# Kernel optimization log

Measured on AMD Instinct MI355X. Metric: run time of the kernel, lower is better.

## Reference

```python
import jax, jax.numpy as jnp
import numpy as np
from jax import lax

B, S, I = 128, 256, 128          # batch, seq_len, input_size
CTX, OUT = 256, 128              # context_input_size, output_size
CPM, NM = 1024, 4                # center_size_per_module, num_modules
CENTER = NM * CPM
IN_SIZES = [I + CTX, CTX, CTX, CTX]          # only module 0 sees the input
HID = [CPM, CPM, CPM, CPM + OUT]             # last module also emits output


def setup_inputs() -> dict:
    key = jax.random.key(0)
    ks = jax.random.split(key, 4 + 5 * NM)
    d = {
        "inputs": jax.random.normal(ks[0], (B, 1, S, I), jnp.float32),
        "center_init": jax.random.normal(ks[1], (NM, B, CPM), jnp.float32),
        "mod_init": jax.random.normal(ks[2], (NM - 1, B, CPM), jnp.float32),
        "mod_init_last": jax.random.normal(ks[3], (B, CPM + OUT), jnp.float32),
    }
    for i in range(NM):
        k = ks[4 + 5 * i: 4 + 5 * (i + 1)]
        d[f"pm{i}"] = jax.random.normal(k[0], (CENTER, CTX), jnp.float32) * 0.02
        d[f"wih{i}"] = jax.random.normal(k[1], (3 * HID[i], IN_SIZES[i]), jnp.float32) * 0.05
        d[f"whh{i}"] = jax.random.normal(k[2], (3 * HID[i], HID[i]), jnp.float32) * 0.05
        d[f"bih{i}"] = jnp.zeros((3 * HID[i],), jnp.float32)
        d[f"bhh{i}"] = jnp.zeros((3 * HID[i],), jnp.float32)
    return d


def _gru(x, h, wih, whh, bih, bhh):
    # PyTorch GRUCell semantics
    gi = x @ wih.T + bih
    gh = h @ whh.T + bhh
    ir, iz, inn = jnp.split(gi, 3, axis=1)
    hr, hz, hn = jnp.split(gh, 3, axis=1)
    r = jax.nn.sigmoid(ir + hr)
    z = jax.nn.sigmoid(iz + hz)
    n = jnp.tanh(inn + r * hn)
    return (1.0 - z) * n + z * h


def _forward(inputs, center_init, mod_init, mod_init_last, pms, wihs, whhs, bihs, bhhs):
    xs = jnp.swapaxes(inputs[:, 0], 0, 1)  # [S, B, I]

    def step(carry, x_t):
        centers, mods, mod_last = carry  # [NM,B,CPM], [NM-1,B,CPM], [B,CPM+OUT]
        # torch.cat(prev_center_states, dim=1): module-major concat -> [B, NM*CPM]
        center_state = jnp.reshape(jnp.swapaxes(centers, 0, 1), (centers.shape[1], -1))
        new_centers, new_mods = [], []
        out = new_mod_last = None
        for i in range(NM):
            ctx = center_state @ pms[i]                       # [B, CTX]
            xin = jnp.concatenate([x_t, ctx], axis=1) if i == 0 else ctx
            h_prev = mod_last if i == NM - 1 else mods[i]
            h = _gru(xin, h_prev, wihs[i], whhs[i], bihs[i], bhhs[i])
            if i == NM - 1:
                out = h[:, :OUT]                              # split([output, center_feat])
                new_centers.append(h[:, OUT:])
                new_mod_last = h
            else:
                new_centers.append(h)
                new_mods.append(h)
        return (jnp.stack(new_centers), jnp.stack(new_mods), new_mod_last), out

    _, ys = lax.scan(step, (center_init, mod_init, mod_init_last), xs)
    return jnp.swapaxes(ys, 0, 1)  # [B, S, OUT]


def reference(inputs, center_init, mod_init, mod_init_last,
              pm0, pm1, pm2, pm3,
              wih0, wih1, wih2, wih3,
              whh0, whh1, whh2, whh3,
              bih0, bih1, bih2, bih3,
              bhh0, bhh1, bhh2, bhh3):
    return _forward(inputs, center_init, mod_init, mod_init_last,
                    (pm0, pm1, pm2, pm3),
                    (wih0, wih1, wih2, wih3),
                    (whh0, whh1, whh2, whh3),
                    (bih0, bih1, bih2, bih3),
                    (bhh0, bhh1, bhh2, bhh3))
```

## Files before the change

### kernel.cpp

```cpp
#include <hip/hip_runtime.h>
#include <hip/hip_bf16.h>

typedef _Float16 f16;
typedef f16  f16x8 __attribute__((ext_vector_type(8)));
typedef float f32x4 __attribute__((ext_vector_type(4)));

__device__ __forceinline__ f16x8 ld8h(const f16* p){ return *reinterpret_cast<const f16x8*>(p); }
__device__ __forceinline__ void fsplit(float x, f16* hi, f16* lo){
    f16 h=(f16)x; *hi=h; *lo=(f16)((x-(float)h)*4096.0f);
}
#define MFMA16(a,b,c) __builtin_amdgcn_mfma_f32_16x16x32_f16((a),(b),(c),0,0,0)
__device__ __forceinline__ size_t fragoff(int n, int k, int Kc){
    return ((size_t)(n>>4)*Kc + (k>>5))*512 + (size_t)((((k&31)>>3)*16 + (n&15))*8 + (k&7));
}

constexpr size_t NXE   = 128ull*256*128;
constexpr size_t NPM   = 1024ull*4096;
constexpr size_t NWIH0 = 3072ull*384;
constexpr size_t NWIH12= 3072ull*256;
constexpr size_t NWIH3 = 3456ull*256;
constexpr size_t NWHH  = 3072ull*1024;
constexpr size_t NWHH3 = 3456ull*1152;
constexpr size_t NCEN  = 128ull*4096;
constexpr size_t NCTX  = 128ull*1024;
constexpr size_t NHMX  = 128ull*1152;

constexpr size_t OFF_XH    = 0;
constexpr size_t OFF_XL    = OFF_XH + NXE*2;
constexpr size_t OFF_PMH   = OFF_XL + NXE*2;
constexpr size_t OFF_PML   = OFF_PMH + NPM*2;
constexpr size_t OFF_WIHH0 = OFF_PML + NPM*2;
constexpr size_t OFF_WIHH1 = OFF_WIHH0 + NWIH0*2;
constexpr size_t OFF_WIHH2 = OFF_WIHH1 + NWIH12*2;
constexpr size_t OFF_WIHH3 = OFF_WIHH2 + NWIH12*2;
constexpr size_t OFF_WIHL0 = OFF_WIHH3 + NWIH3*2;
constexpr size_t OFF_WIHL1 = OFF_WIHL0 + NWIH0*2;
constexpr size_t OFF_WIHL2 = OFF_WIHL1 + NWIH12*2;
constexpr size_t OFF_WIHL3 = OFF_WIHL2 + NWIH12*2;
constexpr size_t OFF_WHHH0 = OFF_WIHL3 + NWIH3*2;
constexpr size_t OFF_WHHH1 = OFF_WHHH0 + NWHH*2;
constexpr size_t OFF_WHHH2 = OFF_WHHH1 + NWHH*2;
constexpr size_t OFF_WHHH3 = OFF_WHHH2 + NWHH*2;
constexpr size_t OFF_WHHL0 = OFF_WHHH3 + NWHH3*2;
constexpr size_t OFF_WHHL1 = OFF_WHHL0 + NWHH*2;
constexpr size_t OFF_WHHL2 = OFF_WHHL1 + NWHH*2;
constexpr size_t OFF_WHHL3 = OFF_WHHL2 + NWHH*2;
constexpr size_t OFF_CENH  = OFF_WHHL3 + NWHH3*2;
constexpr size_t OFF_CENL  = OFF_CENH + 2*NCEN*2;
constexpr size_t OFF_CTXH  = OFF_CENL + 2*NCEN*2;
constexpr size_t OFF_CTXL  = OFF_CTXH + NCTX*2;
constexpr size_t OFF_HH    = OFF_CTXL + NCTX*2;
constexpr size_t OFF_HL    = OFF_HH + 8*NHMX*2;
constexpr size_t OFF_HF    = OFF_HL + 8*NHMX*2;
constexpr size_t WS_NEED   = OFF_HF + 8*NHMX*4;

__device__ __forceinline__ f16* hh_ptr(char* ws,int p,int i){ return (f16*)(ws+OFF_HH+((size_t)(p*4+i))*NHMX*2); }
__device__ __forceinline__ f16* hl_ptr(char* ws,int p,int i){ return (f16*)(ws+OFF_HL+((size_t)(p*4+i))*NHMX*2); }
__device__ __forceinline__ float* hf_ptr(char* ws,int p,int i){ return (float*)(ws+OFF_HF+((size_t)(p*4+i))*NHMX*4); }

__global__ void k_repack_w(const float* __restrict__ src, f16* __restrict__ hi,
                           f16* __restrict__ lo, int K){
    int n = blockIdx.x;
    const float* row = src + (size_t)n*K;
    int Kc = K >> 5;
    for (int k8 = threadIdx.x*8; k8 < K; k8 += 2048) {
        f16x8 hv, lv;
        #pragma unroll
        for (int e = 0; e < 8; ++e) { f16 a,b; fsplit(row[k8+e], &a, &b); hv[e]=a; lv[e]=b; }
        size_t d = fragoff(n, k8, Kc);
        *reinterpret_cast<f16x8*>(hi + d) = hv;
        *reinterpret_cast<f16x8*>(lo + d) = lv;
    }
}

__global__ void k_repack_pm(const float* __restrict__ p0, const float* __restrict__ p1,
                            const float* __restrict__ p2, const float* __restrict__ p3,
                            f16* __restrict__ hi, f16* __restrict__ lo){
    int k0 = blockIdx.x * 8;
    for (int c = threadIdx.x; c < 1024; c += 256) {
        int i = c >> 8, nl = c & 255;
        const float* p = (i==0?p0 : i==1?p1 : i==2?p2 : p3);
        #pragma unroll
        for (int e = 0; e < 8; ++e) {
            f16 a,b; fsplit(p[(size_t)(k0+e)*256 + nl], &a, &b);
            size_t d = fragoff(c, k0+e, 128); hi[d]=a; lo[d]=b;
        }
    }
}

__global__ void k_repack_x(const float* __restrict__ src, f16* __restrict__ hi, f16* __restrict__ lo){
    size_t g = ((size_t)blockIdx.x*256 + threadIdx.x) * 8;
    if (g >= NXE) return;
    int m = (int)(g >> 15), t = (int)((g >> 7) & 255), d0 = (int)(g & 127);
    f16x8 hv, lv;
    #pragma unroll
    for (int e = 0; e < 8; ++e) { f16 a,b; fsplit(src[g+e], &a, &b); hv[e]=a; lv[e]=b; }
    size_t d = (size_t)t*16384 + fragoff(m, d0, 4);
    *reinterpret_cast<f16x8*>(hi + d) = hv;
    *reinterpret_cast<f16x8*>(lo + d) = lv;
}

__global__ void k_init_cen(const float* __restrict__ ci, char* ws){
    size_t g = ((size_t)blockIdx.x*256 + threadIdx.x) * 8;
    if (g >= 4ull*128*1024) return;
    int i = (int)(g >> 17), b = (int)((g >> 10) & 127), c = (int)(g & 1023);
    f16* hi = (f16*)(ws + OFF_CENH);
    f16* lo = (f16*)(ws + OFF_CENL);
    f16x8 hv, lv;
    #pragma unroll
    for (int e = 0; e < 8; ++e) { f16 a,bb; fsplit(ci[g+e], &a, &bb); hv[e]=a; lv[e]=bb; }
    size_t d = fragoff(b, i*1024 + c, 128);
    *reinterpret_cast<f16x8*>(hi + d) = hv;
    *reinterpret_cast<f16x8*>(lo + d) = lv;
}

__global__ void k_init_mod(const float* __restrict__ mi, char* ws){
    size_t g = ((size_t)blockIdx.x*256 + threadIdx.x) * 8;
    if (g >= 3ull*128*1024) return;
    int i = (int)(g >> 17), b = (int)((g >> 10) & 127), j = (int)(g & 1023);
    float* hf = hf_ptr(ws, 0, i);
    f16 *hh = hh_ptr(ws, 0, i), *hl = hl_ptr(ws, 0, i);
    f16x8 hv, lv;
    #pragma unroll
    for (int e = 0; e < 8; ++e) {
        float v = mi[g+e]; hf[(size_t)b*1024 + j + e] = v;
        f16 a,bb; fsplit(v, &a, &bb); hv[e]=a; lv[e]=bb;
    }
    size_t d = fragoff(b, j, 32);
    *reinterpret_cast<f16x8*>(hh + d) = hv;
    *reinterpret_cast<f16x8*>(hl + d) = lv;
}

__global__ void k_init_last(const float* __restrict__ ml, char* ws){
    int b = blockIdx.x;
    float* hf = hf_ptr(ws, 0, 3);
    f16 *hh = hh_ptr(ws, 0, 3), *hl = hl_ptr(ws, 0, 3);
    for (int j = threadIdx.x*8; j < 1152; j += 2048) {
        f16x8 hv, lv;
        #pragma unroll
        for (int e = 0; e < 8; ++e) {
            float v = ml[(size_t)b*1152 + j + e]; hf[(size_t)b*1152 + j + e] = v;
            f16 a,bb; fsplit(v, &a, &bb); hv[e]=a; lv[e]=bb;
        }
        size_t d = fragoff(b, j, 36);
        *reinterpret_cast<f16x8*>(hh + d) = hv;
        *reinterpret_cast<f16x8*>(hl + d) = lv;
    }
}

__global__ __launch_bounds__(512) void k_ctx(char* ws, int par){
    __shared__ float red[8][32][17];
    const f16* cenh = (const f16*)(ws + OFF_CENH) + (size_t)par*NCEN;
    const f16* cenl = (const f16*)(ws + OFF_CENL) + (size_t)par*NCEN;
    const f16* pmh  = (const f16*)(ws + OFF_PMH);
    const f16* pml  = (const f16*)(ws + OFF_PML);
    int tid = threadIdx.x, lane = tid & 63, wv = tid >> 6;
    int bm = blockIdx.x >> 6, bn = blockIdx.x & 63;
    size_t lb = (size_t)lane*8;
    size_t a0 = ((size_t)(bm*2)*128 + wv*16)*512 + lb;
    size_t a1 = a0 + 128*512;
    size_t bb = ((size_t)bn*128 + wv*16)*512 + lb;
    f32x4 h0={},h1={},c0={},c1={};
    #pragma unroll 4
    for (int kc = 0; kc < 16; ++kc) {
        f16x8 bh = ld8h(pmh + bb + kc*512), bl = ld8h(pml + bb + kc*512);
        f16x8 ah0 = ld8h(cenh + a0 + kc*512), al0 = ld8h(cenl + a0 + kc*512);
        f16x8 ah1 = ld8h(cenh + a1 + kc*512), al1 = ld8h(cenl + a1 + kc*512);
        h0 = MFMA16(ah0,bh,h0); c0 = MFMA16(al0,bh,c0); c0 = MFMA16(ah0,bl,c0);
        h1 = MFMA16(ah1,bh,h1); c1 = MFMA16(al1,bh,c1); c1 = MFMA16(ah1,bl,c1);
    }
    int rg = lane >> 4, fr = lane & 15;
    const float inv = 1.0f/4096.0f;
    #pragma unroll
    for (int rr = 0; rr < 4; ++rr) {
        red[wv][rg*4+rr][fr]      = h0[rr] + c0[rr]*inv;
        red[wv][16+rg*4+rr][fr]   = h1[rr] + c1[rr]*inv;
    }
    __syncthreads();
    int r = tid >> 4, c = tid & 15;
    float s = red[0][r][c]+red[1][r][c]+red[2][r][c]+red[3][r][c]
            + red[4][r][c]+red[5][r][c]+red[6][r][c]+red[7][r][c];
    int m = bm*32 + r, n = bn*16 + c;
    size_t d = fragoff(m, n, 32);
    f16* ctxh = (f16*)(ws + OFF_CTXH);
    f16* ctxl = (f16*)(ws + OFF_CTXL);
    fsplit(s, &ctxh[d], &ctxl[d]);
}

__global__ __launch_bounds__(512, 2) void k_fused(char* ws,
    const float* __restrict__ bih0, const float* __restrict__ bih1,
    const float* __restrict__ bih2, const float* __restrict__ bih3,
    const float* __restrict__ bhh0, const float* __restrict__ bhh1,
    const float* __restrict__ bhh2, const float* __restrict__ bhh3,
    float* __restrict__ out, int t, int par)
{
    __shared__ float red[8][4][16][17];
    const int tid = threadIdx.x, lane = tid & 63, wv = tid >> 6;
    const int mp = wv & 3, khalf = wv >> 2;
    const int fr = lane & 15, rg = lane >> 4;
    const int tile = blockIdx.x;
    int i, jt;
    if (tile < 64)       { i = 0; jt = tile; }
    else if (tile < 128) { i = 1; jt = tile - 64; }
    else if (tile < 192) { i = 2; jt = tile - 128; }
    else                 { i = 3; jt = tile - 192; }
    const int H  = (i == 3) ? 1152 : 1024;
    const int K1 = (i == 0) ? 384 : 256;
    const int Kc1 = K1 >> 5, KcH = H >> 5, Ht = H >> 4;
    const int P1h = Kc1 >> 1, PHh = KcH >> 1;

    const f16* WihH = (const f16*)(ws + (i==0?OFF_WIHH0 : i==1?OFF_WIHH1 : i==2?OFF_WIHH2 : OFF_WIHH3));
    const f16* WihL = (const f16*)(ws + (i==0?OFF_WIHL0 : i==1?OFF_WIHL1 : i==2?OFF_WIHL2 : OFF_WIHL3));
    const f16* WhhH = (const f16*)(ws + (i==0?OFF_WHHH0 : i==1?OFF_WHHH1 : i==2?OFF_WHHH2 : OFF_WHHH3));
    const f16* WhhL = (const f16*)(ws + (i==0?OFF_WHHL0 : i==1?OFF_WHHL1 : i==2?OFF_WHHL2 : OFF_WHHL3));

    const size_t lb = (size_t)lane*8;
    size_t b1[3], b2[3];
    #pragma unroll
    for (int s = 0; s < 3; ++s) {
        b1[s] = ((size_t)(s*Ht + jt)*Kc1)*512 + lb;
        b2[s] = ((size_t)(s*Ht + jt)*KcH)*512 + lb;
    }
    const int mt0 = mp*2;

    f32x4 aRh[2]={{},{}}, aRc[2]={{},{}}, aZh[2]={{},{}}, aZc[2]={{},{}};
    f32x4 aIh[2]={{},{}}, aIc[2]={{},{}}, aNh[2]={{},{}}, aNc[2]={{},{}};

    {
        const f16* XH_ = (const f16*)(ws + OFF_XH);
        const f16* XL_ = (const f16*)(ws + OFF_XL);
        const f16* CH_ = (const f16*)(ws + OFF_CTXH);
        const f16* CL_ = (const f16*)(ws + OFF_CTXL);
        size_t xb0 = ((size_t)(t*8 + mt0)*4)*512 + lb, xb1 = xb0 + 2048;
        size_t cb0 = ((size_t)mt0*32)*512 + lb,        cb1 = cb0 + 16384;
        const int kc0 = khalf*P1h, kc1e = kc0 + P1h;
        #pragma unroll 2
        for (int kc = kc0; kc < kc1e; ++kc) {
            f16x8 ah0, al0, ah1, al1;
            if (i == 0 && kc < 4) {
                ah0 = ld8h(XH_ + xb0 + kc*512); al0 = ld8h(XL_ + xb0 + kc*512);
                ah1 = ld8h(XH_ + xb1 + kc*512); al1 = ld8h(XL_ + xb1 + kc*512);
            } else {
                const int ck = (i == 0) ? kc - 4 : i*8 + kc;
                ah0 = ld8h(CH_ + cb0 + ck*512); al0 = ld8h(CL_ + cb0 + ck*512);
                ah1 = ld8h(CH_ + cb1 + ck*512); al1 = ld8h(CL_ + cb1 + ck*512);
            }
            f16x8 bh, bl;
            bh = ld8h(WihH + b1[0] + kc*512); bl = ld8h(WihL + b1[0] + kc*512);
            aRh[0]=MFMA16(ah0,bh,aRh[0]); aRc[0]=MFMA16(al0,bh,aRc[0]); aRc[0]=MFMA16(ah0,bl,aRc[0]);
            aRh[1]=MFMA16(ah1,bh,aRh[1]); aRc[1]=MFMA16(al1,bh,aRc[1]); aRc[1]=MFMA16(ah1,bl,aRc[1]);
            bh = ld8h(WihH + b1[1] + kc*512); bl = ld8h(WihL + b1[1] + kc*512);
            aZh[0]=MFMA16(ah0,bh,aZh[0]); aZc[0]=MFMA16(al0,bh,aZc[0]); aZc[0]=MFMA16(ah0,bl,aZc[0]);
            aZh[1]=MFMA16(ah1,bh,aZh[1]); aZc[1]=MFMA16(al1,bh,aZc[1]); aZc[1]=MFMA16(ah1,bl,aZc[1]);
            bh = ld8h(WihH + b1[2] + kc*512); bl = ld8h(WihL + b1[2] + kc*512);
            aIh[0]=MFMA16(ah0,bh,aIh[0]); aIc[0]=MFMA16(al0,bh,aIc[0]); aIc[0]=MFMA16(ah0,bl,aIc[0]);
            aIh[1]=MFMA16(ah1,bh,aIh[1]); aIc[1]=MFMA16(al1,bh,aIc[1]); aIc[1]=MFMA16(ah1,bl,aIc[1]);
        }
    }
    {
        const f16* HHp = hh_ptr(ws, par, i);
        const f16* HLp = hl_ptr(ws, par, i);
        size_t hb0 = ((size_t)mt0*KcH)*512 + lb, hb1 = hb0 + (size_t)KcH*512;
        const int kc0 = khalf*PHh, kc1e = kc0 + PHh;
        #pragma unroll 2
        for (int kc = kc0; kc < kc1e; ++kc) {
            f16x8 ah0 = ld8h(HHp + hb0 + kc*512), al0 = ld8h(HLp + hb0 + kc*512);
            f16x8 ah1 = ld8h(HHp + hb1 + kc*512), al1 = ld8h(HLp + hb1 + kc*512);
            f16x8 bh, bl;
            bh = ld8h(WhhH + b2[0] + kc*512); bl = ld8h(WhhL + b2[0] + kc*512);
            aRh[0]=MFMA16(ah0,bh,aRh[0]); aRc[0]=MFMA16(al0,bh,aRc[0]); aRc[0]=MFMA16(ah0,bl,aRc[0]);
            aRh[1]=MFMA16(ah1,bh,aRh[1]); aRc[1]=MFMA16(al1,bh,aRc[1]); aRc[1]=MFMA16(ah1,bl,aRc[1]);
            bh = ld8h(WhhH + b2[1] + kc*512); bl = ld8h(WhhL + b2[1] + kc*512);
            aZh[0]=MFMA16(ah0,bh,aZh[0]); aZc[0]=MFMA16(al0,bh,aZc[0]); aZc[0]=MFMA16(ah0,bl,aZc[0]);
            aZh[1]=MFMA16(ah1,bh,aZh[1]); aZc[1]=MFMA16(al1,bh,aZc[1]); aZc[1]=MFMA16(ah1,bl,aZc[1]);
            bh = ld8h(WhhH + b2[2] + kc*512); bl = ld8h(WhhL + b2[2] + kc*512);
            aNh[0]=MFMA16(ah0,bh,aNh[0]); aNc[0]=MFMA16(al0,bh,aNc[0]); aNc[0]=MFMA16(ah0,bl,aNc[0]);
            aNh[1]=MFMA16(ah1,bh,aNh[1]); aNc[1]=MFMA16(al1,bh,aNc[1]); aNc[1]=MFMA16(ah1,bl,aNc[1]);
        }
    }

    const float inv = 1.0f/4096.0f;
    if (khalf == 1) {
        #pragma unroll
        for (int mi = 0; mi < 2; ++mi) {
            const int mt = mt0 + mi, r16 = rg*4;
            #pragma unroll
            for (int rr = 0; rr < 4; ++rr) {
                red[mt][0][r16+rr][fr] = aRh[mi][rr] + aRc[mi][rr]*inv;
                red[mt][1][r16+rr][fr] = aZh[mi][rr] + aZc[mi][rr]*inv;
                red[mt][2][r16+rr][fr] = aIh[mi][rr] + aIc[mi][rr]*inv;
                red[mt][3][r16+rr][fr] = aNh[mi][rr] + aNc[mi][rr]*inv;
            }
        }
    }
    __syncthreads();
    if (khalf == 1) return;

    const float* bihp = (i==0?bih0 : i==1?bih1 : i==2?bih2 : bih3);
    const float* bhhp = (i==0?bhh0 : i==1?bhh1 : i==2?bhh2 : bhh3);
    const int j = jt*16 + fr;
    const float bir = bihp[j], biz = bihp[H+j], bin = bihp[2*H+j];
    const float bhr = bhhp[j], bhz = bhhp[H+j], bhn = bhhp[2*H+j];
    const float* hfP = hf_ptr(ws, par, i);
    float* hfN = hf_ptr(ws, par^1, i);
    f16 *hhN = hh_ptr(ws, par^1, i), *hlN = hl_ptr(ws, par^1, i);
    f16* cenhN = (f16*)(ws + OFF_CENH) + (size_t)(par^1)*NCEN;
    f16* cenlN = (f16*)(ws + OFF_CENL) + (size_t)(par^1)*NCEN;
    #pragma unroll
    for (int mi = 0; mi < 2; ++mi) {
        const int mt = mt0 + mi, r16 = rg*4;
        #pragma unroll
        for (int rr = 0; rr < 4; ++rr) {
            float r_  = aRh[mi][rr] + aRc[mi][rr]*inv + red[mt][0][r16+rr][fr] + bir + bhr;
            float z_  = aZh[mi][rr] + aZc[mi][rr]*inv + red[mt][1][r16+rr][fr] + biz + bhz;
            float in_ = aIh[mi][rr] + aIc[mi][rr]*inv + red[mt][2][r16+rr][fr] + bin;
            float hn_ = aNh[mi][rr] + aNc[mi][rr]*inv + red[mt][3][r16+rr][fr] + bhn;
            float rgt = 1.f/(1.f + expf(-r_));
            float zgt = 1.f/(1.f + expf(-z_));
            float ngt = tanhf(in_ + rgt*hn_);
            int m = mt*16 + rg*4 + rr;
            float hp = hfP[(size_t)m*H + j];
            float hnew = (1.f - zgt)*ngt + zgt*hp;
            hfN[(size_t)m*H + j] = hnew;
            size_t hd = fragoff(m, j, KcH);
            fsplit(hnew, &hhN[hd], &hlN[hd]);
            if (i < 3) {
                size_t cd = fragoff(m, i*1024 + j, 128);
                fsplit(hnew, &cenhN[cd], &cenlN[cd]);
            } else if (j >= 128) {
                size_t cd = fragoff(m, 3072 + j - 128, 128);
                fsplit(hnew, &cenhN[cd], &cenlN[cd]);
            } else {
                out[((size_t)m*256 + t)*128 + j] = hnew;
            }
        }
    }
}

extern "C" void kernel_launch(void* const* d_in, const int* in_sizes, int n_in,
                              void* d_out, int out_size, void* d_ws, size_t ws_size,
                              hipStream_t stream)
{
    char* ws = (char*)d_ws;
    const float* inp   = (const float*)d_in[0];
    const float* cini  = (const float*)d_in[1];
    const float* mini  = (const float*)d_in[2];
    const float* mlast = (const float*)d_in[3];
    const float *pm[4], *wih[4], *whh[4], *bih[4], *bhh[4];
    for (int i = 0; i < 4; ++i) {
        pm[i]  = (const float*)d_in[4 + 5*i];
        wih[i] = (const float*)d_in[5 + 5*i];
        whh[i] = (const float*)d_in[6 + 5*i];
        bih[i] = (const float*)d_in[7 + 5*i];
        bhh[i] = (const float*)d_in[8 + 5*i];
    }
    float* out = (float*)d_out;

    k_repack_x<<<2048, 256, 0, stream>>>(inp, (f16*)(ws+OFF_XH), (f16*)(ws+OFF_XL));
    k_repack_pm<<<512, 256, 0, stream>>>(pm[0], pm[1], pm[2], pm[3],
                                         (f16*)(ws+OFF_PMH), (f16*)(ws+OFF_PML));
    k_repack_w<<<3072, 256, 0, stream>>>(wih[0], (f16*)(ws+OFF_WIHH0), (f16*)(ws+OFF_WIHL0), 384);
    k_repack_w<<<3072, 256, 0, stream>>>(wih[1], (f16*)(ws+OFF_WIHH1), (f16*)(ws+OFF_WIHL1), 256);
    k_repack_w<<<3072, 256, 0, stream>>>(wih[2], (f16*)(ws+OFF_WIHH2), (f16*)(ws+OFF_WIHL2), 256);
    k_repack_w<<<3456, 256, 0, stream>>>(wih[3], (f16*)(ws+OFF_WIHH3), (f16*)(ws+OFF_WIHL3), 256);
    k_repack_w<<<3072, 256, 0, stream>>>(whh[0], (f16*)(ws+OFF_WHHH0), (f16*)(ws+OFF_WHHL0), 1024);
    k_repack_w<<<3072, 256, 0, stream>>>(whh[1], (f16*)(ws+OFF_WHHH1), (f16*)(ws+OFF_WHHL1), 1024);
    k_repack_w<<<3072, 256, 0, stream>>>(whh[2], (f16*)(ws+OFF_WHHH2), (f16*)(ws+OFF_WHHL2), 1024);
    k_repack_w<<<3456, 256, 0, stream>>>(whh[3], (f16*)(ws+OFF_WHHH3), (f16*)(ws+OFF_WHHL3), 1152);
    k_init_cen<<<256, 256, 0, stream>>>(cini, ws);
    k_init_mod<<<192, 256, 0, stream>>>(mini, ws);
    k_init_last<<<128, 256, 0, stream>>>(mlast, ws);

    for (int t = 0; t < 256; ++t) {
        int par = t & 1;
        k_ctx<<<256, 512, 0, stream>>>(ws, par);
        k_fused<<<264, 512, 0, stream>>>(ws,
            bih[0], bih[1], bih[2], bih[3],
            bhh[0], bhh[1], bhh[2], bhh[3],
            out, t, par);
    }
    (void)in_sizes; (void)n_in; (void)out_size; (void)ws_size; (void)WS_NEED;
}
```

Before: 12.60 ms.

## Split fused GRU kernel across batch halves and four-way K split

```diff
diff --git a/kernel.cpp b/kernel.cpp
--- a/kernel.cpp
+++ b/kernel.cpp
@@ -187,18 +187,18 @@
     fsplit(s, &ctxh[d], &ctxl[d]);
 }
 
-__global__ __launch_bounds__(512, 2) void k_fused(char* ws,
+__global__ __launch_bounds__(512, 4) void k_fused(char* ws,
     const float* __restrict__ bih0, const float* __restrict__ bih1,
     const float* __restrict__ bih2, const float* __restrict__ bih3,
     const float* __restrict__ bhh0, const float* __restrict__ bhh1,
     const float* __restrict__ bhh2, const float* __restrict__ bhh3,
     float* __restrict__ out, int t, int par)
 {
-    __shared__ float red[8][4][16][17];
+    __shared__ float red[4][4][16][17];
     const int tid = threadIdx.x, lane = tid & 63, wv = tid >> 6;
-    const int mp = wv & 3, khalf = wv >> 2;
+    const int mp = wv & 1, kq = wv >> 1;
     const int fr = lane & 15, rg = lane >> 4;
-    const int tile = blockIdx.x;
+    const int tile = blockIdx.x >> 1, rh = blockIdx.x & 1;
     int i, jt;
     if (tile < 64)       { i = 0; jt = tile; }
     else if (tile < 128) { i = 1; jt = tile - 64; }
@@ -207,7 +207,7 @@
     const int H  = (i == 3) ? 1152 : 1024;
     const int K1 = (i == 0) ? 384 : 256;
     const int Kc1 = K1 >> 5, KcH = H >> 5, Ht = H >> 4;
-    const int P1h = Kc1 >> 1, PHh = KcH >> 1;
+    const int P1q = Kc1 >> 2, PHq = KcH >> 2;
 
     const f16* WihH = (const f16*)(ws + (i==0?OFF_WIHH0 : i==1?OFF_WIHH1 : i==2?OFF_WIHH2 : OFF_WIHH3));
     const f16* WihL = (const f16*)(ws + (i==0?OFF_WIHL0 : i==1?OFF_WIHL1 : i==2?OFF_WIHL2 : OFF_WIHL3));
@@ -221,7 +221,7 @@
         b1[s] = ((size_t)(s*Ht + jt)*Kc1)*512 + lb;
         b2[s] = ((size_t)(s*Ht + jt)*KcH)*512 + lb;
     }
-    const int mt0 = mp*2;
+    const int mt0 = rh*4 + mp*2;
 
     f32x4 aRh[2]={{},{}}, aRc[2]={{},{}}, aZh[2]={{},{}}, aZc[2]={{},{}};
     f32x4 aIh[2]={{},{}}, aIc[2]={{},{}}, aNh[2]={{},{}}, aNc[2]={{},{}};
@@ -233,7 +233,7 @@
         const f16* CL_ = (const f16*)(ws + OFF_CTXL);
         size_t xb0 = ((size_t)(t*8 + mt0)*4)*512 + lb, xb1 = xb0 + 2048;
         size_t cb0 = ((size_t)mt0*32)*512 + lb,        cb1 = cb0 + 16384;
-        const int kc0 = khalf*P1h, kc1e = kc0 + P1h;
+        const int kc0 = kq*P1q, kc1e = kc0 + P1q;
         #pragma unroll 2
         for (int kc = kc0; kc < kc1e; ++kc) {
             f16x8 ah0, al0, ah1, al1;
@@ -261,7 +261,7 @@
         const f16* HHp = hh_ptr(ws, par, i);
         const f16* HLp = hl_ptr(ws, par, i);
         size_t hb0 = ((size_t)mt0*KcH)*512 + lb, hb1 = hb0 + (size_t)KcH*512;
-        const int kc0 = khalf*PHh, kc1e = kc0 + PHh;
+        const int kc0 = kq*PHq, kc1e = kc0 + PHq;
         #pragma unroll 2
         for (int kc = kc0; kc < kc1e; ++kc) {
             f16x8 ah0 = ld8h(HHp + hb0 + kc*512), al0 = ld8h(HLp + hb0 + kc*512);
@@ -280,21 +280,50 @@
     }
 
     const float inv = 1.0f/4096.0f;
-    if (khalf == 1) {
+    const int r16 = rg*4;
+    if (kq == 3) {
         #pragma unroll
         for (int mi = 0; mi < 2; ++mi) {
-            const int mt = mt0 + mi, r16 = rg*4;
+            const int lm = mp*2 + mi;
             #pragma unroll
             for (int rr = 0; rr < 4; ++rr) {
-                red[mt][0][r16+rr][fr] = aRh[mi][rr] + aRc[mi][rr]*inv;
-                red[mt][1][r16+rr][fr] = aZh[mi][rr] + aZc[mi][rr]*inv;
-                red[mt][2][r16+rr][fr] = aIh[mi][rr] + aIc[mi][rr]*inv;
-                red[mt][3][r16+rr][fr] = aNh[mi][rr] + aNc[mi][rr]*inv;
+                red[lm][0][r16+rr][fr] = aRh[mi][rr] + aRc[mi][rr]*inv;
+                red[lm][1][r16+rr][fr] = aZh[mi][rr] + aZc[mi][rr]*inv;
+                red[lm][2][r16+rr][fr] = aIh[mi][rr] + aIc[mi][rr]*inv;
+                red[lm][3][r16+rr][fr] = aNh[mi][rr] + aNc[mi][rr]*inv;
             }
         }
     }
     __syncthreads();
-    if (khalf == 1) return;
+    if (kq == 2) {
+        #pragma unroll
+        for (int mi = 0; mi < 2; ++mi) {
+            const int lm = mp*2 + mi;
+            #pragma unroll
+            for (int rr = 0; rr < 4; ++rr) {
+                red[lm][0][r16+rr][fr] += aRh[mi][rr] + aRc[mi][rr]*inv;
+                red[lm][1][r16+rr][fr] += aZh[mi][rr] + aZc[mi][rr]*inv;
+                red[lm][2][r16+rr][fr] += aIh[mi][rr] + aIc[mi][rr]*inv;
+                red[lm][3][r16+rr][fr] += aNh[mi][rr] + aNc[mi][rr]*inv;
+            }
+        }
+    }
+    __syncthreads();
+    if (kq == 1) {
+        #pragma unroll
+        for (int mi = 0; mi < 2; ++mi) {
+            const int lm = mp*2 + mi;
+            #pragma unroll
+            for (int rr = 0; rr < 4; ++rr) {
+                red[lm][0][r16+rr][fr] += aRh[mi][rr] + aRc[mi][rr]*inv;
+                red[lm][1][r16+rr][fr] += aZh[mi][rr] + aZc[mi][rr]*inv;
+                red[lm][2][r16+rr][fr] += aIh[mi][rr] + aIc[mi][rr]*inv;
+                red[lm][3][r16+rr][fr] += aNh[mi][rr] + aNc[mi][rr]*inv;
+            }
+        }
+    }
+    __syncthreads();
+    if (kq != 0) return;
 
     const float* bihp = (i==0?bih0 : i==1?bih1 : i==2?bih2 : bih3);
     const float* bhhp = (i==0?bhh0 : i==1?bhh1 : i==2?bhh2 : bhh3);
@@ -308,17 +337,17 @@
     f16* cenlN = (f16*)(ws + OFF_CENL) + (size_t)(par^1)*NCEN;
     #pragma unroll
     for (int mi = 0; mi < 2; ++mi) {
-        const int mt = mt0 + mi, r16 = rg*4;
+        const int lm = mp*2 + mi;
         #pragma unroll
         for (int rr = 0; rr < 4; ++rr) {
-            float r_  = aRh[mi][rr] + aRc[mi][rr]*inv + red[mt][0][r16+rr][fr] + bir + bhr;
-            float z_  = aZh[mi][rr] + aZc[mi][rr]*inv + red[mt][1][r16+rr][fr] + biz + bhz;
-            float in_ = aIh[mi][rr] + aIc[mi][rr]*inv + red[mt][2][r16+rr][fr] + bin;
-            float hn_ = aNh[mi][rr] + aNc[mi][rr]*inv + red[mt][3][r16+rr][fr] + bhn;
+            float r_  = aRh[mi][rr] + aRc[mi][rr]*inv + red[lm][0][r16+rr][fr] + bir + bhr;
+            float z_  = aZh[mi][rr] + aZc[mi][rr]*inv + red[lm][1][r16+rr][fr] + biz + bhz;
+            float in_ = aIh[mi][rr] + aIc[mi][rr]*inv + red[lm][2][r16+rr][fr] + bin;
+            float hn_ = aNh[mi][rr] + aNc[mi][rr]*inv + red[lm][3][r16+rr][fr] + bhn;
             float rgt = 1.f/(1.f + expf(-r_));
             float zgt = 1.f/(1.f + expf(-z_));
             float ngt = tanhf(in_ + rgt*hn_);
-            int m = mt*16 + rg*4 + rr;
+            int m = (mt0 + mi)*16 + r16 + rr;
             float hp = hfP[(size_t)m*H + j];
             float hnew = (1.f - zgt)*ngt + zgt*hp;
             hfN[(size_t)m*H + j] = hnew;
@@ -374,7 +403,7 @@
     for (int t = 0; t < 256; ++t) {
         int par = t & 1;
         k_ctx<<<256, 512, 0, stream>>>(ws, par);
-        k_fused<<<264, 512, 0, stream>>>(ws,
+        k_fused<<<528, 512, 0, stream>>>(ws,
             bih[0], bih[1], bih[2], bih[3],
             bhh[0], bhh[1], bhh[2], bhh[3],
             out, t, par);
```

New measurement: 16.56 ms. 1.31x slower.

## Drop separate center and fp32 state buffers; split GRU tiles across more blocks

Applied to the files above, without the earlier changes.

```diff
diff --git a/kernel.cpp b/kernel.cpp
--- a/kernel.cpp
+++ b/kernel.cpp
@@ -21,7 +21,6 @@
 constexpr size_t NWIH3 = 3456ull*256;
 constexpr size_t NWHH  = 3072ull*1024;
 constexpr size_t NWHH3 = 3456ull*1152;
-constexpr size_t NCEN  = 128ull*4096;
 constexpr size_t NCTX  = 128ull*1024;
 constexpr size_t NHMX  = 128ull*1152;
 
@@ -45,18 +44,16 @@
 constexpr size_t OFF_WHHL1 = OFF_WHHL0 + NWHH*2;
 constexpr size_t OFF_WHHL2 = OFF_WHHL1 + NWHH*2;
 constexpr size_t OFF_WHHL3 = OFF_WHHL2 + NWHH*2;
-constexpr size_t OFF_CENH  = OFF_WHHL3 + NWHH3*2;
-constexpr size_t OFF_CENL  = OFF_CENH + 2*NCEN*2;
-constexpr size_t OFF_CTXH  = OFF_CENL + 2*NCEN*2;
+constexpr size_t OFF_C0H   = OFF_WHHL3 + NWHH3*2;
+constexpr size_t OFF_C0L   = OFF_C0H + 4*NHMX*2;
+constexpr size_t OFF_CTXH  = OFF_C0L + 4*NHMX*2;
 constexpr size_t OFF_CTXL  = OFF_CTXH + NCTX*2;
 constexpr size_t OFF_HH    = OFF_CTXL + NCTX*2;
 constexpr size_t OFF_HL    = OFF_HH + 8*NHMX*2;
-constexpr size_t OFF_HF    = OFF_HL + 8*NHMX*2;
-constexpr size_t WS_NEED   = OFF_HF + 8*NHMX*4;
+constexpr size_t WS_NEED   = OFF_HL + 8*NHMX*2;
 
 __device__ __forceinline__ f16* hh_ptr(char* ws,int p,int i){ return (f16*)(ws+OFF_HH+((size_t)(p*4+i))*NHMX*2); }
 __device__ __forceinline__ f16* hl_ptr(char* ws,int p,int i){ return (f16*)(ws+OFF_HL+((size_t)(p*4+i))*NHMX*2); }
-__device__ __forceinline__ float* hf_ptr(char* ws,int p,int i){ return (float*)(ws+OFF_HF+((size_t)(p*4+i))*NHMX*4); }
 
 __global__ void k_repack_w(const float* __restrict__ src, f16* __restrict__ hi,
                            f16* __restrict__ lo, int K){
@@ -104,12 +101,12 @@
     size_t g = ((size_t)blockIdx.x*256 + threadIdx.x) * 8;
     if (g >= 4ull*128*1024) return;
     int i = (int)(g >> 17), b = (int)((g >> 10) & 127), c = (int)(g & 1023);
-    f16* hi = (f16*)(ws + OFF_CENH);
-    f16* lo = (f16*)(ws + OFF_CENL);
+    f16* hi = (f16*)(ws + OFF_C0H) + (size_t)i*NHMX;
+    f16* lo = (f16*)(ws + OFF_C0L) + (size_t)i*NHMX;
     f16x8 hv, lv;
     #pragma unroll
     for (int e = 0; e < 8; ++e) { f16 a,bb; fsplit(ci[g+e], &a, &bb); hv[e]=a; lv[e]=bb; }
-    size_t d = fragoff(b, i*1024 + c, 128);
+    size_t d = (i < 3) ? fragoff(b, c, 32) : fragoff(b, 128 + c, 36);
     *reinterpret_cast<f16x8*>(hi + d) = hv;
     *reinterpret_cast<f16x8*>(lo + d) = lv;
 }
@@ -118,14 +115,10 @@
     size_t g = ((size_t)blockIdx.x*256 + threadIdx.x) * 8;
     if (g >= 3ull*128*1024) return;
     int i = (int)(g >> 17), b = (int)((g >> 10) & 127), j = (int)(g & 1023);
-    float* hf = hf_ptr(ws, 0, i);
     f16 *hh = hh_ptr(ws, 0, i), *hl = hl_ptr(ws, 0, i);
     f16x8 hv, lv;
     #pragma unroll
-    for (int e = 0; e < 8; ++e) {
-        float v = mi[g+e]; hf[(size_t)b*1024 + j + e] = v;
-        f16 a,bb; fsplit(v, &a, &bb); hv[e]=a; lv[e]=bb;
-    }
+    for (int e = 0; e < 8; ++e) { f16 a,bb; fsplit(mi[g+e], &a, &bb); hv[e]=a; lv[e]=bb; }
     size_t d = fragoff(b, j, 32);
     *reinterpret_cast<f16x8*>(hh + d) = hv;
     *reinterpret_cast<f16x8*>(hl + d) = lv;
@@ -133,39 +126,44 @@
 
 __global__ void k_init_last(const float* __restrict__ ml, char* ws){
     int b = blockIdx.x;
-    float* hf = hf_ptr(ws, 0, 3);
     f16 *hh = hh_ptr(ws, 0, 3), *hl = hl_ptr(ws, 0, 3);
     for (int j = threadIdx.x*8; j < 1152; j += 2048) {
         f16x8 hv, lv;
         #pragma unroll
-        for (int e = 0; e < 8; ++e) {
-            float v = ml[(size_t)b*1152 + j + e]; hf[(size_t)b*1152 + j + e] = v;
-            f16 a,bb; fsplit(v, &a, &bb); hv[e]=a; lv[e]=bb;
-        }
+        for (int e = 0; e < 8; ++e) { f16 a,bb; fsplit(ml[(size_t)b*1152 + j + e], &a, &bb); hv[e]=a; lv[e]=bb; }
         size_t d = fragoff(b, j, 36);
         *reinterpret_cast<f16x8*>(hh + d) = hv;
         *reinterpret_cast<f16x8*>(hl + d) = lv;
     }
 }
 
-__global__ __launch_bounds__(512) void k_ctx(char* ws, int par){
+__global__ __launch_bounds__(512) void k_ctx(char* ws, int par, int t){
     __shared__ float red[8][32][17];
-    const f16* cenh = (const f16*)(ws + OFF_CENH) + (size_t)par*NCEN;
-    const f16* cenl = (const f16*)(ws + OFF_CENL) + (size_t)par*NCEN;
     const f16* pmh  = (const f16*)(ws + OFF_PMH);
     const f16* pml  = (const f16*)(ws + OFF_PML);
     int tid = threadIdx.x, lane = tid & 63, wv = tid >> 6;
     int bm = blockIdx.x >> 6, bn = blockIdx.x & 63;
+    int mod = wv >> 1, half = wv & 1;
+    const int Kc_m = (mod == 3) ? 36 : 32;
+    const int koff = ((mod == 3) ? 4 : 0) + half*16;
+    const f16 *Ah, *Al;
+    if (t == 0) {
+        Ah = (const f16*)(ws + OFF_C0H) + (size_t)mod*NHMX;
+        Al = (const f16*)(ws + OFF_C0L) + (size_t)mod*NHMX;
+    } else {
+        Ah = hh_ptr(ws, par, mod);
+        Al = hl_ptr(ws, par, mod);
+    }
     size_t lb = (size_t)lane*8;
-    size_t a0 = ((size_t)(bm*2)*128 + wv*16)*512 + lb;
-    size_t a1 = a0 + 128*512;
+    size_t a0 = ((size_t)(bm*2)*Kc_m + koff)*512 + lb;
+    size_t a1 = a0 + (size_t)Kc_m*512;
     size_t bb = ((size_t)bn*128 + wv*16)*512 + lb;
     f32x4 h0={},h1={},c0={},c1={};
     #pragma unroll 4
     for (int kc = 0; kc < 16; ++kc) {
         f16x8 bh = ld8h(pmh + bb + kc*512), bl = ld8h(pml + bb + kc*512);
-        f16x8 ah0 = ld8h(cenh + a0 + kc*512), al0 = ld8h(cenl + a0 + kc*512);
-        f16x8 ah1 = ld8h(cenh + a1 + kc*512), al1 = ld8h(cenl + a1 + kc*512);
+        f16x8 ah0 = ld8h(Ah + a0 + kc*512), al0 = ld8h(Al + a0 + kc*512);
+        f16x8 ah1 = ld8h(Ah + a1 + kc*512), al1 = ld8h(Al + a1 + kc*512);
         h0 = MFMA16(ah0,bh,h0); c0 = MFMA16(al0,bh,c0); c0 = MFMA16(ah0,bl,c0);
         h1 = MFMA16(ah1,bh,h1); c1 = MFMA16(al1,bh,c1); c1 = MFMA16(ah1,bl,c1);
     }
@@ -194,11 +192,11 @@
     const float* __restrict__ bhh2, const float* __restrict__ bhh3,
     float* __restrict__ out, int t, int par)
 {
-    __shared__ float red[8][4][16][17];
+    __shared__ float red[3][4][64][17];
     const int tid = threadIdx.x, lane = tid & 63, wv = tid >> 6;
-    const int mp = wv & 3, khalf = wv >> 2;
+    const int kq = wv & 3, mp = wv >> 2;
     const int fr = lane & 15, rg = lane >> 4;
-    const int tile = blockIdx.x;
+    const int tile = blockIdx.x >> 1, rh = blockIdx.x & 1;
     int i, jt;
     if (tile < 64)       { i = 0; jt = tile; }
     else if (tile < 128) { i = 1; jt = tile - 64; }
@@ -207,7 +205,7 @@
     const int H  = (i == 3) ? 1152 : 1024;
     const int K1 = (i == 0) ? 384 : 256;
     const int Kc1 = K1 >> 5, KcH = H >> 5, Ht = H >> 4;
-    const int P1h = Kc1 >> 1, PHh = KcH >> 1;
+    const int P1q = Kc1 >> 2, PHq = KcH >> 2;
 
     const f16* WihH = (const f16*)(ws + (i==0?OFF_WIHH0 : i==1?OFF_WIHH1 : i==2?OFF_WIHH2 : OFF_WIHH3));
     const f16* WihL = (const f16*)(ws + (i==0?OFF_WIHL0 : i==1?OFF_WIHL1 : i==2?OFF_WIHL2 : OFF_WIHL3));
@@ -221,7 +219,7 @@
         b1[s] = ((size_t)(s*Ht + jt)*Kc1)*512 + lb;
         b2[s] = ((size_t)(s*Ht + jt)*KcH)*512 + lb;
     }
-    const int mt0 = mp*2;
+    const int mt0 = rh*4 + mp*2;
 
     f32x4 aRh[2]={{},{}}, aRc[2]={{},{}}, aZh[2]={{},{}}, aZc[2]={{},{}};
     f32x4 aIh[2]={{},{}}, aIc[2]={{},{}}, aNh[2]={{},{}}, aNc[2]={{},{}};
@@ -233,7 +231,7 @@
         const f16* CL_ = (const f16*)(ws + OFF_CTXL);
         size_t xb0 = ((size_t)(t*8 + mt0)*4)*512 + lb, xb1 = xb0 + 2048;
         size_t cb0 = ((size_t)mt0*32)*512 + lb,        cb1 = cb0 + 16384;
-        const int kc0 = khalf*P1h, kc1e = kc0 + P1h;
+        const int kc0 = kq*P1q, kc1e = kc0 + P1q;
         #pragma unroll 2
         for (int kc = kc0; kc < kc1e; ++kc) {
             f16x8 ah0, al0, ah1, al1;
@@ -261,7 +259,7 @@
         const f16* HHp = hh_ptr(ws, par, i);
         const f16* HLp = hl_ptr(ws, par, i);
         size_t hb0 = ((size_t)mt0*KcH)*512 + lb, hb1 = hb0 + (size_t)KcH*512;
-        const int kc0 = khalf*PHh, kc1e = kc0 + PHh;
+        const int kc0 = kq*PHq, kc1e = kc0 + PHq;
         #pragma unroll 2
         for (int kc = kc0; kc < kc1e; ++kc) {
             f16x8 ah0 = ld8h(HHp + hb0 + kc*512), al0 = ld8h(HLp + hb0 + kc*512);
@@ -280,59 +278,54 @@
     }
 
     const float inv = 1.0f/4096.0f;
-    if (khalf == 1) {
+    const int r16 = rg*4;
+    if (kq != 0) {
         #pragma unroll
         for (int mi = 0; mi < 2; ++mi) {
-            const int mt = mt0 + mi, r16 = rg*4;
             #pragma unroll
             for (int rr = 0; rr < 4; ++rr) {
-                red[mt][0][r16+rr][fr] = aRh[mi][rr] + aRc[mi][rr]*inv;
-                red[mt][1][r16+rr][fr] = aZh[mi][rr] + aZc[mi][rr]*inv;
-                red[mt][2][r16+rr][fr] = aIh[mi][rr] + aIc[mi][rr]*inv;
-                red[mt][3][r16+rr][fr] = aNh[mi][rr] + aNc[mi][rr]*inv;
+                const int row = mp*32 + mi*16 + r16 + rr;
+                red[kq-1][0][row][fr] = aRh[mi][rr] + aRc[mi][rr]*inv;
+                red[kq-1][1][row][fr] = aZh[mi][rr] + aZc[mi][rr]*inv;
+                red[kq-1][2][row][fr] = aIh[mi][rr] + aIc[mi][rr]*inv;
+                red[kq-1][3][row][fr] = aNh[mi][rr] + aNc[mi][rr]*inv;
             }
         }
     }
     __syncthreads();
-    if (khalf == 1) return;
+    if (kq != 0) return;
 
     const float* bihp = (i==0?bih0 : i==1?bih1 : i==2?bih2 : bih3);
     const float* bhhp = (i==0?bhh0 : i==1?bhh1 : i==2?bhh2 : bhh3);
     const int j = jt*16 + fr;
     const float bir = bihp[j], biz = bihp[H+j], bin = bihp[2*H+j];
     const float bhr = bhhp[j], bhz = bhhp[H+j], bhn = bhhp[2*H+j];
-    const float* hfP = hf_ptr(ws, par, i);
-    float* hfN = hf_ptr(ws, par^1, i);
+    const f16* hhP = hh_ptr(ws, par, i);
+    const f16* hlP = hl_ptr(ws, par, i);
     f16 *hhN = hh_ptr(ws, par^1, i), *hlN = hl_ptr(ws, par^1, i);
-    f16* cenhN = (f16*)(ws + OFF_CENH) + (size_t)(par^1)*NCEN;
-    f16* cenlN = (f16*)(ws + OFF_CENL) + (size_t)(par^1)*NCEN;
     #pragma unroll
     for (int mi = 0; mi < 2; ++mi) {
-        const int mt = mt0 + mi, r16 = rg*4;
         #pragma unroll
         for (int rr = 0; rr < 4; ++rr) {
-            float r_  = aRh[mi][rr] + aRc[mi][rr]*inv + red[mt][0][r16+rr][fr] + bir + bhr;
-            float z_  = aZh[mi][rr] + aZc[mi][rr]*inv + red[mt][1][r16+rr][fr] + biz + bhz;
-            float in_ = aIh[mi][rr] + aIc[mi][rr]*inv + red[mt][2][r16+rr][fr] + bin;
-            float hn_ = aNh[mi][rr] + aNc[mi][rr]*inv + red[mt][3][r16+rr][fr] + bhn;
+            const int row = mp*32 + mi*16 + r16 + rr;
+            float r_  = aRh[mi][rr] + aRc[mi][rr]*inv
+                      + red[0][0][row][fr] + red[1][0][row][fr] + red[2][0][row][fr] + bir + bhr;
+            float z_  = aZh[mi][rr] + aZc[mi][rr]*inv
+                      + red[0][1][row][fr] + red[1][1][row][fr] + red[2][1][row][fr] + biz + bhz;
+            float in_ = aIh[mi][rr] + aIc[mi][rr]*inv
+                      + red[0][2][row][fr] + red[1][2][row][fr] + red[2][2][row][fr] + bin;
+            float hn_ = aNh[mi][rr] + aNc[mi][rr]*inv
+                      + red[0][3][row][fr] + red[1][3][row][fr] + red[2][3][row][fr] + bhn;
             float rgt = 1.f/(1.f + expf(-r_));
             float zgt = 1.f/(1.f + expf(-z_));
             float ngt = tanhf(in_ + rgt*hn_);
-            int m = mt*16 + rg*4 + rr;
-            float hp = hfP[(size_t)m*H + j];
+            const int m = rh*64 + row;
+            size_t hd = fragoff(m, j, KcH);
+            float hp = (float)hhP[hd] + (float)hlP[hd]*inv;
             float hnew = (1.f - zgt)*ngt + zgt*hp;
-            hfN[(size_t)m*H + j] = hnew;
-            size_t hd = fragoff(m, j, KcH);
             fsplit(hnew, &hhN[hd], &hlN[hd]);
-            if (i < 3) {
-                size_t cd = fragoff(m, i*1024 + j, 128);
-                fsplit(hnew, &cenhN[cd], &cenlN[cd]);
-            } else if (j >= 128) {
-                size_t cd = fragoff(m, 3072 + j - 128, 128);
-                fsplit(hnew, &cenhN[cd], &cenlN[cd]);
-            } else {
+            if (i == 3 && j < 128)
                 out[((size_t)m*256 + t)*128 + j] = hnew;
-            }
         }
     }
 }
@@ -373,8 +366,8 @@
 
     for (int t = 0; t < 256; ++t) {
         int par = t & 1;
-        k_ctx<<<256, 512, 0, stream>>>(ws, par);
-        k_fused<<<264, 512, 0, stream>>>(ws,
+        k_ctx<<<256, 512, 0, stream>>>(ws, par, t);
+        k_fused<<<528, 512, 0, stream>>>(ws,
             bih[0], bih[1], bih[2], bih[3],
             bhh[0], bhh[1], bhh[2], bhh[3],
             out, t, par);
```

Result: no change. 12.58 ms (-0.1%).
